# Optimization experiments

Hardware: AMD Instinct MI355X
Metric: run time of the kernel (lower is better)

Reference implementation:

```python
import jax, jax.numpy as jnp
import numpy as np
import math

HIDDEN = 2048
NUM_HEADS = 32
NUM_KV_HEADS = 8
HEAD_DIM = HIDDEN // NUM_HEADS
GROUPS = NUM_HEADS // NUM_KV_HEADS
B, S = 2, 2048


def setup_inputs() -> dict:
    key = jax.random.key(0)
    ks = jax.random.split(key, 9)
    sc = 1.0 / math.sqrt(HIDDEN)
    x = jax.random.normal(ks[0], (B, S, HIDDEN), dtype=jnp.float32)
    # causal mask: 1 where attention allowed, 0 where masked
    mask = jnp.tril(jnp.ones((S, S), dtype=jnp.int32))[None, None, :, :]
    Wq = jax.random.normal(ks[1], (HIDDEN, HIDDEN), dtype=jnp.float32) * sc
    bq = jnp.zeros((HIDDEN,), dtype=jnp.float32)
    Wk = jax.random.normal(ks[2], (NUM_KV_HEADS * HEAD_DIM, HIDDEN), dtype=jnp.float32) * sc
    bk = jnp.zeros((NUM_KV_HEADS * HEAD_DIM,), dtype=jnp.float32)
    Wv = jax.random.normal(ks[3], (NUM_KV_HEADS * HEAD_DIM, HIDDEN), dtype=jnp.float32) * sc
    bv = jnp.zeros((NUM_KV_HEADS * HEAD_DIM,), dtype=jnp.float32)
    Wo = jax.random.normal(ks[4], (HIDDEN, HIDDEN), dtype=jnp.float32) * sc
    bo = jnp.zeros((HIDDEN,), dtype=jnp.float32)
    return {"x": x, "mask": mask, "Wq": Wq, "bq": bq, "Wk": Wk, "bk": bk,
            "Wv": Wv, "bv": bv, "Wo": Wo, "bo": bo}


def reference(x, mask, Wq, bq, Wk, bk, Wv, bv, Wo, bo):
    b, s, _ = x.shape
    # projections (torch Linear: y = x @ W.T + b)
    Q = (x @ Wq.T + bq).reshape(b, s, NUM_HEADS, HEAD_DIM).transpose(0, 2, 1, 3)  # b h s d
    K = (x @ Wk.T + bk).reshape(b, s, NUM_KV_HEADS, HEAD_DIM).transpose(0, 2, 1, 3)
    V = (x @ Wv.T + bv).reshape(b, s, NUM_KV_HEADS, HEAD_DIM).transpose(0, 2, 1, 3)
    # repeat_kv expansion
    K = jnp.repeat(K, GROUPS, axis=1)  # b h s d
    V = jnp.repeat(V, GROUPS, axis=1)
    scores = jnp.einsum('bhqd,bhkd->bhqk', Q, K) / math.sqrt(HEAD_DIM)
    scores = jnp.where(mask == 0, jnp.float32(-jnp.inf), scores)
    w = jax.nn.softmax(scores, axis=-1)
    # dropout is identity in eval mode
    out = jnp.einsum('bhqk,bhkd->bhqd', w, V)
    out = out.transpose(0, 2, 1, 3).reshape(b, s, HIDDEN)
    return out @ Wo.T + bo
```

## Files before the change

### kernel.cpp

```cpp
#include <hip/hip_runtime.h>
#include <hip/hip_bf16.h>
#include <stdint.h>

#define HID   2048
#define SLEN  2048
#define NB    2
#define NHEADS 32
#define NKVH   8
#define HDIM   64
#define KVW    512

typedef __bf16 bf16_t;
typedef __bf16 bf16x2 __attribute__((ext_vector_type(2)));
typedef __bf16 bf16x4 __attribute__((ext_vector_type(4)));
typedef __bf16 bf16x8 __attribute__((ext_vector_type(8)));
typedef float  f32x4  __attribute__((ext_vector_type(4)));

__device__ __forceinline__ f32x4 mfma16(bf16x8 a, bf16x8 b, f32x4 c) {
  return __builtin_amdgcn_mfma_f32_16x16x32_bf16(a, b, c, 0, 0, 0);
}

__device__ __forceinline__ void gl2lds16(const bf16_t* g, bf16_t* l) {
  __builtin_amdgcn_global_load_lds(
      (const __attribute__((address_space(1))) void*)g,
      (__attribute__((address_space(3))) void*)l,
      16, 0, 0);
}

__device__ __forceinline__ float fast_exp2(float x) {
#if __has_builtin(__builtin_amdgcn_exp2f)
  return __builtin_amdgcn_exp2f(x);
#else
  return __expf(x * 0.69314718f);
#endif
}

__device__ __forceinline__ bf16x8 ld8(const bf16_t* p) {
  return *(const bf16x8*)p;
}
__device__ __forceinline__ bf16x8 ld8(const float* p) {
  f32x4 a = *(const f32x4*)p;
  f32x4 b = *(const f32x4*)(p + 4);
  bf16x8 r;
  r[0] = (bf16_t)a[0]; r[1] = (bf16_t)a[1]; r[2] = (bf16_t)a[2]; r[3] = (bf16_t)a[3];
  r[4] = (bf16_t)b[0]; r[5] = (bf16_t)b[1]; r[6] = (bf16_t)b[2]; r[7] = (bf16_t)b[3];
  return r;
}

__device__ __forceinline__ uint32_t pack2(float a, float b) {
  bf16x2 t; t[0] = (bf16_t)a; t[1] = (bf16_t)b;
  return __builtin_bit_cast(uint32_t, t);
}

__device__ __forceinline__ void st_c(bf16_t* p, float v) { *p = (bf16_t)v; }
__device__ __forceinline__ void st_c(float*  p, float v) { *p = v; }

__global__ __launch_bounds__(256) void cvt_kernel(
    const float* __restrict__ x,  const float* __restrict__ wq,
    const float* __restrict__ wk, const float* __restrict__ wv,
    const float* __restrict__ wo,
    const float* __restrict__ bq, const float* __restrict__ bk,
    const float* __restrict__ bv,
    bf16_t* xb, bf16_t* wqb, bf16_t* wkb, bf16_t* wvb, bf16_t* wob,
    float* bcat)
{
  if (blockIdx.y >= 5) {
    const float* fs; float* fd; size_t n;
    if (blockIdx.y == 5)      { fs = bq; fd = bcat;        n = HID; }
    else if (blockIdx.y == 6) { fs = bk; fd = bcat + HID;  n = KVW; }
    else                      { fs = bv; fd = bcat + HID + KVW; n = KVW; }
    const size_t stride4 = (size_t)gridDim.x * 256 * 4;
    for (size_t i = ((size_t)blockIdx.x * 256 + threadIdx.x) * 4; i < n; i += stride4)
      *(f32x4*)(fd + i) = *(const f32x4*)(fs + i);
    return;
  }
  const float* s; bf16_t* d; size_t n;
  switch (blockIdx.y) {
    case 0:  s = x;  d = xb;  n = (size_t)NB * SLEN * HID; break;
    case 1:  s = wq; d = wqb; n = (size_t)HID * HID; break;
    case 2:  s = wk; d = wkb; n = (size_t)KVW * HID; break;
    case 3:  s = wv; d = wvb; n = (size_t)KVW * HID; break;
    default: s = wo; d = wob; n = (size_t)HID * HID; break;
  }
  const size_t stride = (size_t)gridDim.x * 256 * 8;
  for (size_t i = ((size_t)blockIdx.x * 256 + threadIdx.x) * 8; i < n; i += stride)
    *(bf16x8*)(d + i) = ld8(s + i);
}

__device__ __forceinline__ bf16x8 ldfrag(const bf16_t* __restrict__ Lh, int r, int g) {
  return *(const bf16x8*)(Lh + r * 64 + ((g ^ (r & 7)) << 3));
}

template <int Q>
__device__ __forceinline__ void mfma_quad(const bf16x8 (&af)[2][2],
                                          const bf16x8 (&bfr)[4][2],
                                          f32x4 (&acc)[8][4]) {
#pragma unroll
  for (int ks = 0; ks < 2; ++ks)
#pragma unroll
    for (int i = 0; i < 2; ++i)
#pragma unroll
      for (int ni = 0; ni < 4; ++ni)
        acc[2 * Q + i][ni] = mfma16(af[i][ks], bfr[ni][ks], acc[2 * Q + i][ni]);
}

__device__ __forceinline__ void phase_barrier() {
  __builtin_amdgcn_s_barrier();
  asm volatile("" ::: "memory");
}

__device__ __forceinline__ void gemm256_core(
    const bf16_t* __restrict__ Ag,
    const bf16_t* __restrict__ Bg,
    bf16_t* __restrict__ lds, f32x4 (&acc)[8][4])
{
  const int tid  = threadIdx.x;
  const int lane = tid & 63;
  const int w    = tid >> 6;
  const int fr   = lane & 15;
  const int quad = lane >> 4;
  const int wr   = w >> 2;
  const int wc   = w & 3;
  const int rbB  = (wc & 1) * 64;

  bf16_t* A0 = lds;
  bf16_t* B0 = lds + 16384;
  bf16_t* A1 = lds + 32768;
  bf16_t* B1 = lds + 49152;
  const bf16_t* Ar0 = A0 + wr * 8192;
  const bf16_t* Br0 = B0 + (wc >> 1) * 8192;
  const bf16_t* Ar1 = A1 + wr * 8192;
  const bf16_t* Br1 = B1 + (wc >> 1) * 8192;

  const f32x4 z4 = {0.f, 0.f, 0.f, 0.f};
#pragma unroll
  for (int i = 0; i < 8; ++i)
#pragma unroll
    for (int j = 0; j < 4; ++j) acc[i][j] = z4;

  auto STAGE = [&](const bf16_t* __restrict__ Gp, bf16_t* __restrict__ Lh) {
#pragma unroll
    for (int j = 0; j < 2; ++j) {
      const int s = j * 512 + tid;
      const int r = s >> 3;
      const int g = (s & 7) ^ (r & 7);
      gl2lds16(Gp + (size_t)r * HID + g * 8, Lh + s * 8);
    }
  };

  STAGE(Bg,                  B0);
  STAGE(Bg + 128 * HID,      B0 + 8192);
  STAGE(Ag,                  A0);
  STAGE(Ag + 128 * HID,      A0 + 8192);
  STAGE(Bg + 64,             B1);
  STAGE(Bg + 128 * HID + 64, B1 + 8192);
  asm volatile("s_waitcnt vmcnt(4)" ::: "memory");
  phase_barrier();

  bf16x8 bfr[4][2], af[2][2];

#pragma unroll 1
  for (int it = 0; it < 16; ++it) {
    const bool more = (it < 15);
    const size_t k1 = (size_t)(2 * it + 1) * 64;
    const size_t k2 = (size_t)(2 * it + 2) * 64;
    const size_t k3 = (size_t)(2 * it + 3) * 64;

#pragma unroll
    for (int ni = 0; ni < 4; ++ni)
#pragma unroll
      for (int ks = 0; ks < 2; ++ks)
        bfr[ni][ks] = ldfrag(Br0, rbB + ni * 16 + fr, ks * 4 + quad);
#pragma unroll
    for (int i = 0; i < 2; ++i)
#pragma unroll
      for (int ks = 0; ks < 2; ++ks)
        af[i][ks] = ldfrag(Ar0, i * 16 + fr, ks * 4 + quad);
    STAGE(Ag + k1, A1);
    phase_barrier();
    asm volatile("s_waitcnt lgkmcnt(0)" ::: "memory");
    __builtin_amdgcn_s_setprio(1);
    mfma_quad<0>(af, bfr, acc);
    __builtin_amdgcn_s_setprio(0);
    phase_barrier();

#pragma unroll
    for (int i = 0; i < 2; ++i)
#pragma unroll
      for (int ks = 0; ks < 2; ++ks)
        af[i][ks] = ldfrag(Ar0, 32 + i * 16 + fr, ks * 4 + quad);
    STAGE(Ag + 128 * HID + k1, A1 + 8192);
    phase_barrier();
    asm volatile("s_waitcnt lgkmcnt(0)" ::: "memory");
    __builtin_amdgcn_s_setprio(1);
    mfma_quad<1>(af, bfr, acc);
    __builtin_amdgcn_s_setprio(0);
    phase_barrier();

#pragma unroll
    for (int i = 0; i < 2; ++i)
#pragma unroll
      for (int ks = 0; ks < 2; ++ks)
        af[i][ks] = ldfrag(Ar0, 64 + i * 16 + fr, ks * 4 + quad);
    if (more) STAGE(Bg + k2, B0);
    phase_barrier();
    asm volatile("s_waitcnt lgkmcnt(0)" ::: "memory");
    __builtin_amdgcn_s_setprio(1);
    mfma_quad<2>(af, bfr, acc);
    __builtin_amdgcn_s_setprio(0);
    phase_barrier();

#pragma unroll
    for (int i = 0; i < 2; ++i)
#pragma unroll
      for (int ks = 0; ks < 2; ++ks)
        af[i][ks] = ldfrag(Ar0, 96 + i * 16 + fr, ks * 4 + quad);
    if (more) STAGE(Bg + 128 * HID + k2, B0 + 8192);
    phase_barrier();
    asm volatile("s_waitcnt lgkmcnt(0)" ::: "memory");
    __builtin_amdgcn_s_setprio(1);
    mfma_quad<3>(af, bfr, acc);
    __builtin_amdgcn_s_setprio(0);
    if (more) { asm volatile("s_waitcnt vmcnt(4)" ::: "memory"); }
    else      { asm volatile("s_waitcnt vmcnt(0)" ::: "memory"); }
    phase_barrier();

#pragma unroll
    for (int ni = 0; ni < 4; ++ni)
#pragma unroll
      for (int ks = 0; ks < 2; ++ks)
        bfr[ni][ks] = ldfrag(Br1, rbB + ni * 16 + fr, ks * 4 + quad);
#pragma unroll
    for (int i = 0; i < 2; ++i)
#pragma unroll
      for (int ks = 0; ks < 2; ++ks)
        af[i][ks] = ldfrag(Ar1, i * 16 + fr, ks * 4 + quad);
    if (more) STAGE(Ag + k2, A0);
    phase_barrier();
    asm volatile("s_waitcnt lgkmcnt(0)" ::: "memory");
    __builtin_amdgcn_s_setprio(1);
    mfma_quad<0>(af, bfr, acc);
    __builtin_amdgcn_s_setprio(0);
    phase_barrier();

#pragma unroll
    for (int i = 0; i < 2; ++i)
#pragma unroll
      for (int ks = 0; ks < 2; ++ks)
        af[i][ks] = ldfrag(Ar1, 32 + i * 16 + fr, ks * 4 + quad);
    if (more) STAGE(Ag + 128 * HID + k2, A0 + 8192);
    phase_barrier();
    asm volatile("s_waitcnt lgkmcnt(0)" ::: "memory");
    __builtin_amdgcn_s_setprio(1);
    mfma_quad<1>(af, bfr, acc);
    __builtin_amdgcn_s_setprio(0);
    phase_barrier();

#pragma unroll
    for (int i = 0; i < 2; ++i)
#pragma unroll
      for (int ks = 0; ks < 2; ++ks)
        af[i][ks] = ldfrag(Ar1, 64 + i * 16 + fr, ks * 4 + quad);
    if (more) STAGE(Bg + k3, B1);
    phase_barrier();
    asm volatile("s_waitcnt lgkmcnt(0)" ::: "memory");
    __builtin_amdgcn_s_setprio(1);
    mfma_quad<2>(af, bfr, acc);
    __builtin_amdgcn_s_setprio(0);
    phase_barrier();

#pragma unroll
    for (int i = 0; i < 2; ++i)
#pragma unroll
      for (int ks = 0; ks < 2; ++ks)
        af[i][ks] = ldfrag(Ar1, 96 + i * 16 + fr, ks * 4 + quad);
    if (more) STAGE(Bg + 128 * HID + k3, B1 + 8192);
    phase_barrier();
    asm volatile("s_waitcnt lgkmcnt(0)" ::: "memory");
    __builtin_amdgcn_s_setprio(1);
    mfma_quad<3>(af, bfr, acc);
    __builtin_amdgcn_s_setprio(0);
    if (more) { asm volatile("s_waitcnt vmcnt(4)" ::: "memory"); }
    phase_barrier();
  }
}

__global__ __launch_bounds__(512, 2) void qkv8_kernel(
    const bf16_t* __restrict__ xb, const bf16_t* __restrict__ Wcat,
    const float* __restrict__ bcat,
    bf16_t* __restrict__ Qb, bf16_t* __restrict__ Kb, bf16_t* __restrict__ VbT)
{
  __shared__ __align__(16) bf16_t lds[65536];
  const int cb = blockIdx.x;
  const int mb = blockIdx.y;
  f32x4 acc[8][4];
  gemm256_core(xb + (size_t)mb * 256 * HID, Wcat + (size_t)cb * 256 * HID, lds, acc);

  const int tid = threadIdx.x, lane = tid & 63, w = tid >> 6;
  const int fr = lane & 15, quad = lane >> 4, wr = w >> 2, wc = w & 3;
#pragma unroll
  for (int ni = 0; ni < 4; ++ni) {
    const int gcol = cb * 256 + wc * 64 + ni * 16 + fr;
    const float bz = bcat[gcol];
#pragma unroll
    for (int mi = 0; mi < 8; ++mi) {
      const int grow = mb * 256 + wr * 128 + mi * 16 + quad * 4;
      if (cb < 8) {
#pragma unroll
        for (int r = 0; r < 4; ++r)
          Qb[(size_t)(grow + r) * HID + gcol] = (bf16_t)(acc[mi][ni][r] + bz);
      } else if (cb < 10) {
        const int kc = gcol - 2048;
#pragma unroll
        for (int r = 0; r < 4; ++r)
          Kb[(size_t)(grow + r) * KVW + kc] = (bf16_t)(acc[mi][ni][r] + bz);
      } else {
        const int vc = gcol - 2560;
        const int b = grow >> 11, s = grow & 2047;
        bf16x4 pk;
#pragma unroll
        for (int r = 0; r < 4; ++r) pk[r] = (bf16_t)(acc[mi][ni][r] + bz);
        *(bf16x4*)&VbT[((size_t)(b * NKVH + (vc >> 6)) * HDIM + (vc & 63)) * SLEN + s] = pk;
      }
    }
  }
}

__global__ __launch_bounds__(512, 2) void oproj8_kernel(
    const bf16_t* __restrict__ A, const bf16_t* __restrict__ Wob,
    const float* __restrict__ bo, float* __restrict__ out)
{
  __shared__ __align__(16) bf16_t lds[65536];
  const int cb = blockIdx.x;
  const int mb = blockIdx.y;
  f32x4 acc[8][4];
  gemm256_core(A + (size_t)mb * 256 * HID, Wob + (size_t)cb * 256 * HID, lds, acc);

  const int tid = threadIdx.x, lane = tid & 63, w = tid >> 6;
  const int fr = lane & 15, quad = lane >> 4, wr = w >> 2, wc = w & 3;
#pragma unroll
  for (int ni = 0; ni < 4; ++ni) {
    const int gcol = cb * 256 + wc * 64 + ni * 16 + fr;
    const float bz = bo[gcol];
#pragma unroll
    for (int mi = 0; mi < 8; ++mi) {
      const int grow = mb * 256 + wr * 128 + mi * 16 + quad * 4;
#pragma unroll
      for (int r = 0; r < 4; ++r)
        out[(size_t)(grow + r) * HID + gcol] = acc[mi][ni][r] + bz;
    }
  }
}

template <typename AT, typename CT>
__device__ __forceinline__ void gemm128_tile(
    const AT* __restrict__ Ap, int lda,
    const float* __restrict__ Wp, int ldw,
    const float* __restrict__ biasp,
    CT* __restrict__ Cp, int ldc,
    int K)
{
  __shared__ __align__(16) bf16_t Al[128 * 32];
  __shared__ __align__(16) bf16_t Bl[128 * 32];

  const int tid  = threadIdx.x;
  const int lane = tid & 63;
  const int w    = tid >> 6;
  const int fr   = lane & 15;
  const int quad = lane >> 4;
  const int wm   = (w >> 1) * 64;
  const int wn   = (w & 1) * 64;

  const f32x4 z4 = {0.f, 0.f, 0.f, 0.f};
  f32x4 acc[4][4];
  for (int i = 0; i < 4; ++i)
    for (int j = 0; j < 4; ++j) acc[i][j] = z4;

  const int c0    = w * 2;
  const int srow0 = lane >> 2;
  const int skc   = (lane & 3) * 8;

  for (int k0 = 0; k0 < K; k0 += 32) {
    bf16x8 av[2], bv[2];
    for (int t = 0; t < 2; ++t) {
      const int r = (c0 + t) * 16 + srow0;
      av[t] = ld8(Ap + (size_t)r * lda + k0 + skc);
      bv[t] = ld8(Wp + (size_t)r * ldw + k0 + skc);
    }
    for (int t = 0; t < 2; ++t) {
      const int c = c0 + t;
      *(bf16x8*)&Al[c * 512 + lane * 8] = av[t];
      *(bf16x8*)&Bl[c * 512 + lane * 8] = bv[t];
    }
    __syncthreads();
    bf16x8 af[4], bfr[4];
    for (int mi = 0; mi < 4; ++mi)
      af[mi] = *(const bf16x8*)&Al[(wm + mi * 16 + fr) * 32 + quad * 8];
    for (int ni = 0; ni < 4; ++ni)
      bfr[ni] = *(const bf16x8*)&Bl[(wn + ni * 16 + fr) * 32 + quad * 8];
    for (int mi = 0; mi < 4; ++mi)
      for (int ni = 0; ni < 4; ++ni)
        acc[mi][ni] = mfma16(af[mi], bfr[ni], acc[mi][ni]);
    __syncthreads();
  }

  for (int ni = 0; ni < 4; ++ni) {
    const int col = wn + ni * 16 + fr;
    const float bz = biasp[col];
    for (int mi = 0; mi < 4; ++mi) {
      const int r0 = wm + mi * 16 + quad * 4;
      for (int r = 0; r < 4; ++r)
        st_c(Cp + (size_t)(r0 + r) * ldc + col, acc[mi][ni][r] + bz);
    }
  }
}

__global__ __launch_bounds__(256) void qkv_kernel(
    const float* __restrict__ x,
    const float* __restrict__ Wq, const float* __restrict__ bq,
    const float* __restrict__ Wk, const float* __restrict__ bk,
    const float* __restrict__ Wv, const float* __restrict__ bv,
    bf16_t* Qb, bf16_t* Kb, bf16_t* Vb)
{
  const int nb = blockIdx.x;
  const int mb = blockIdx.y;
  const float* W; const float* bias; bf16_t* C; int ldc;
  if (nb < 16)      { W = Wq + (size_t)nb * 128 * HID;  bias = bq + nb * 128;
                      C = Qb + nb * 128; ldc = HID; }
  else if (nb < 20) { const int j = nb - 16;
                      W = Wk + (size_t)j * 128 * HID;   bias = bk + j * 128;
                      C = Kb + j * 128; ldc = KVW; }
  else              { const int j = nb - 20;
                      W = Wv + (size_t)j * 128 * HID;   bias = bv + j * 128;
                      C = Vb + j * 128; ldc = KVW; }
  gemm128_tile<float, bf16_t>(x + (size_t)mb * 128 * HID, HID, W, HID, bias,
                              C + (size_t)mb * 128 * ldc, ldc, HID);
}

__global__ __launch_bounds__(256) void oproj_kernel(
    const bf16_t* __restrict__ A, const float* __restrict__ Wo,
    const float* __restrict__ bo, float* out)
{
  const int nb = blockIdx.x, mb = blockIdx.y;
  gemm128_tile<bf16_t, float>(A + (size_t)mb * 128 * HID, HID,
                              Wo + (size_t)nb * 128 * HID, HID,
                              bo + nb * 128,
                              out + (size_t)mb * 128 * HID + nb * 128, HID, HID);
}

__global__ __launch_bounds__(256) void vtrans_kernel(
    const bf16_t* __restrict__ Vb, bf16_t* __restrict__ VbT)
{
  __shared__ bf16_t T[64][72];
  const int st = blockIdx.x, kvh = blockIdx.y, b = blockIdx.z;
  const int tid = threadIdx.x;
  {
    const int row = tid >> 2;
    const int c16 = (tid & 3) * 16;
    const bf16_t* src =
        Vb + ((size_t)b * SLEN + st * 64 + row) * KVW + kvh * HDIM + c16;
    *(bf16x8*)&T[row][c16]     = *(const bf16x8*)(src);
    *(bf16x8*)&T[row][c16 + 8] = *(const bf16x8*)(src + 8);
  }
  __syncthreads();
  {
    const int d  = tid >> 2;
    const int sc = (tid & 3) * 16;
    bf16_t tmp[16];
    for (int j = 0; j < 16; ++j) tmp[j] = T[sc + j][d];
    bf16_t* dst = VbT + ((size_t)(b * NKVH + kvh) * HDIM + d) * SLEN + st * 64 + sc;
    *(bf16x8*)dst       = *(bf16x8*)&tmp[0];
    *(bf16x8*)(dst + 8) = *(bf16x8*)&tmp[8];
  }
}

__global__ __launch_bounds__(256, 4) void attn_kernel(
    const bf16_t* Q, const bf16_t* __restrict__ Kg,
    const bf16_t* __restrict__ VT, bf16_t* O)
{
  const int bid = blockIdx.x;
  const int xcd = bid & 7;
  const int j   = bid >> 3;
  const int kvh = xcd;
  const int b   = j >> 6;
  const int rem = j & 63;
  const int h   = kvh * 4 + (rem & 3);
  const int pid = rem >> 2;

  const int tid  = threadIdx.x;
  const int lane = tid & 63;
  const int w    = tid >> 6;
  const int fr   = lane & 15;
  const int quad = lane >> 4;

  __shared__ __align__(16) bf16_t KL[8192];
  __shared__ __align__(16) bf16_t VtL[8192];

  const size_t qbase = (size_t)b * SLEN;
  const bf16_t* VTh = VT + (size_t)(b * NKVH + kvh) * HDIM * SLEN;

  const int sig = ((quad & 1) << 1) | ((quad >> 1) & 1);
  const int fsw = (fr >> 1) & 3;
  const bool oddq = (quad & 1);

  bf16x8 ones8;
  {
    const bf16_t o1 = (bf16_t)(fr == 0 ? 1.0f : 0.0f);
#pragma unroll
    for (int j2 = 0; j2 < 8; ++j2) ones8[j2] = o1;
  }

  for (int half = 0; half < 2; ++half) {
    const int qt = half ? (31 - pid) : pid;
    const int q0 = qt * 64;

    bf16x8 qf[2];
#pragma unroll
    for (int ks = 0; ks < 2; ++ks)
      qf[ks] = *(const bf16x8*)&Q[(qbase + q0 + w * 16 + fr) * HID
                                  + h * HDIM + ks * 32 + quad * 8];

    const f32x4 z4 = {0.f, 0.f, 0.f, 0.f};
    f32x4 o_acc[4];
    f32x4 o_l = z4;
#pragma unroll
    for (int di = 0; di < 4; ++di) o_acc[di] = z4;

    const int ktmax = qt >> 1;
    const int qloc  = (qt & 1) * 64 + w * 16 + fr;

    for (int kt = 0; kt <= ktmax; ++kt) {
      const size_t krow0 = qbase + (size_t)kt * 128;

#pragma unroll
      for (int jj = 0; jj < 4; ++jj) {
        const int s  = jj * 256 + tid;
        const int ks = s >> 9, kr = (s >> 2) & 127, c8 = (s & 3) ^ ((kr >> 1) & 3);
        gl2lds16(&Kg[(krow0 + kr) * KVW + kvh * HDIM + ks * 32 + c8 * 8],
                 &KL[s * 8]);
      }
#pragma unroll
      for (int jj = 0; jj < 4; ++jj) {
        const int idx = jj * 256 + tid;
        const int kb = idx >> 8, d = (idx >> 2) & 63, c8 = (idx & 3) ^ ((d >> 1) & 3);
        gl2lds16(&VTh[(size_t)d * SLEN + kt * 128 + kb * 32 + c8 * 8],
                 &VtL[idx * 8]);
      }
      __syncthreads();

      f32x4 s8[8];
#pragma unroll
      for (int ki = 0; ki < 8; ++ki) s8[ki] = z4;
#pragma unroll
      for (int ks = 0; ks < 2; ++ks)
#pragma unroll
        for (int ki = 0; ki < 8; ++ki) {
          bf16x8 kf = *(const bf16x8*)&KL[ks * 4096 + (ki * 16 + fr) * 32
                                          + ((quad ^ fsw) << 3)];
          s8[ki] = mfma16(kf, qf[ks], s8[ki]);
        }

      const float C2 = 0.18033688f;
      const bool diag = (kt == ktmax);

#pragma unroll
      for (int m = 0; m < 4; ++m) {
        float pe[8];
#pragma unroll
        for (int ki2 = 0; ki2 < 2; ++ki2) {
          const int ki = 2 * m + ki2;
#pragma unroll
          for (int r = 0; r < 4; ++r) {
            float p = fast_exp2(s8[ki][r] * C2);
            if (diag && (ki * 16 + quad * 4 + r > qloc)) p = 0.f;
            pe[ki2 * 4 + r] = p;
          }
        }
        uint32_t pw0 = pack2(pe[0], pe[1]);
        uint32_t pw1 = pack2(pe[2], pe[3]);
        uint32_t pw2 = pack2(pe[4], pe[5]);
        uint32_t pw3 = pack2(pe[6], pe[7]);
        uint32_t x0 = oddq ? pw0 : pw2;
        uint32_t x1 = oddq ? pw1 : pw3;
        uint32_t r0 = (uint32_t)__shfl_xor((int)x0, 16);
        uint32_t r1 = (uint32_t)__shfl_xor((int)x1, 16);
        union { uint32_t u[4]; bf16x8 v; } pb;
        pb.u[0] = oddq ? r0 : pw0;
        pb.u[1] = oddq ? r1 : pw1;
        pb.u[2] = oddq ? pw2 : r0;
        pb.u[3] = oddq ? pw3 : r1;

        o_l = mfma16(pb.v, ones8, o_l);
#pragma unroll
        for (int di = 0; di < 4; ++di) {
          bf16x8 vf = *(const bf16x8*)&VtL[m * 2048 + (di * 16 + fr) * 32
                                           + ((sig ^ fsw) << 3)];
          o_acc[di] = mfma16(pb.v, vf, o_acc[di]);
        }
      }
      __syncthreads();
    }

#pragma unroll
    for (int r = 0; r < 4; ++r) {
      const float l  = __shfl(o_l[r], lane & 48);
      const float rl = 1.f / l;
      const size_t qg = qbase + q0 + w * 16 + quad * 4 + r;
#pragma unroll
      for (int di = 0; di < 4; ++di)
        O[qg * HID + h * HDIM + di * 16 + fr] = (bf16_t)(o_acc[di][r] * rl);
    }
  }
}

extern "C" void kernel_launch(void* const* d_in, const int* in_sizes, int n_in,
                              void* d_out, int out_size, void* d_ws, size_t ws_size,
                              hipStream_t stream) {
  const float* x  = (const float*)d_in[0];
  const float* Wq = (const float*)d_in[2];
  const float* bq = (const float*)d_in[3];
  const float* Wk = (const float*)d_in[4];
  const float* bk = (const float*)d_in[5];
  const float* Wv = (const float*)d_in[6];
  const float* bv = (const float*)d_in[7];
  const float* Wo = (const float*)d_in[8];
  const float* bo = (const float*)d_in[9];
  float* out = (float*)d_out;

  const size_t M = (size_t)NB * SLEN;
  dim3 blk(256, 1, 1);

  const size_t needA = (M * HID
                        + (size_t)HID * HID
                        + (size_t)KVW * HID
                        + (size_t)KVW * HID
                        + (size_t)HID * HID
                        + M * HID
                        + M * KVW
                        + M * KVW) * 2
                       + (size_t)(HID + 2 * KVW) * sizeof(float);
  if (ws_size >= needA) {
    bf16_t* xb  = (bf16_t*)d_ws;
    bf16_t* Wqb = xb  + M * HID;
    bf16_t* Wkb = Wqb + (size_t)HID * HID;
    bf16_t* Wvb = Wkb + (size_t)KVW * HID;
    bf16_t* Wob = Wvb + (size_t)KVW * HID;
    bf16_t* Qb  = Wob + (size_t)HID * HID;
    bf16_t* Kb  = Qb  + M * HID;
    bf16_t* VbT = Kb  + M * KVW;
    float*  bcat = (float*)(VbT + M * KVW);

    cvt_kernel<<<dim3(1024, 8, 1), blk, 0, stream>>>(
        x, Wq, Wk, Wv, Wo, bq, bk, bv, xb, Wqb, Wkb, Wvb, Wob, bcat);
    qkv8_kernel<<<dim3(12, 16, 1), dim3(512, 1, 1), 0, stream>>>(
        xb, Wqb, bcat, Qb, Kb, VbT);
    attn_kernel<<<dim3(1024, 1, 1), blk, 0, stream>>>(Qb, Kb, VbT, Qb);
    oproj8_kernel<<<dim3(8, 16, 1), dim3(512, 1, 1), 0, stream>>>(
        Qb, Wob, bo, out);
  } else {
    bf16_t* Qb  = (bf16_t*)d_ws;
    bf16_t* Kb  = Qb + M * KVW * 0 + M * HID;
    bf16_t* Vb  = Kb + M * KVW;
    bf16_t* VbT = Vb + M * KVW;

    qkv_kernel<<<dim3(24, 32, 1), blk, 0, stream>>>(x, Wq, bq, Wk, bk, Wv, bv, Qb, Kb, Vb);
    vtrans_kernel<<<dim3(32, 8, 2), blk, 0, stream>>>(Vb, VbT);
    attn_kernel<<<dim3(1024, 1, 1), blk, 0, stream>>>(Qb, Kb, VbT, Qb);
    oproj_kernel<<<dim3(16, 32, 1), blk, 0, stream>>>(Qb, Wo, bo, out);
  }
}
```

Before: 320.6 us.

## Double-buffer K/V tiles in attention with 512-thread blocks and staged output stores

The attention kernel now uses 512-thread blocks that each own a 128-row query tile, halving the grid. K and V^T tiles are double-buffered in one 64 KB LDS array, so the next tile's global-to-LDS load overlaps the current tile's MFMA work, with one barrier per iteration instead of two. MFMA sections are wrapped in s_setprio, and the output is staged through LDS so global writes are coalesced 16-element vectors. The larger LDS footprint and block size lower occupancy, and the coarser causal tiles add some masked work on the diagonal.

```diff
diff --git a/kernel.cpp b/kernel.cpp
--- a/kernel.cpp
+++ b/kernel.cpp
@@ -474,16 +474,15 @@
   }
 }
 
-__global__ __launch_bounds__(256, 4) void attn_kernel(
+__global__ __launch_bounds__(512, 4) void attn_kernel(
     const bf16_t* Q, const bf16_t* __restrict__ Kg,
     const bf16_t* __restrict__ VT, bf16_t* O)
 {
   const int bid = blockIdx.x;
-  const int xcd = bid & 7;
-  const int j   = bid >> 3;
-  const int kvh = xcd;
-  const int b   = j >> 6;
-  const int rem = j & 63;
+  const int kvh = bid & 7;
+  const int jb  = bid >> 3;
+  const int b   = jb >> 5;
+  const int rem = jb & 31;
   const int h   = kvh * 4 + (rem & 3);
   const int pid = rem >> 2;
 
@@ -493,8 +492,7 @@
   const int fr   = lane & 15;
   const int quad = lane >> 4;
 
-  __shared__ __align__(16) bf16_t KL[8192];
-  __shared__ __align__(16) bf16_t VtL[8192];
+  __shared__ __align__(16) bf16_t lds[32768];
 
   const size_t qbase = (size_t)b * SLEN;
   const bf16_t* VTh = VT + (size_t)(b * NKVH + kvh) * HDIM * SLEN;
@@ -510,9 +508,28 @@
     for (int j2 = 0; j2 < 8; ++j2) ones8[j2] = o1;
   }
 
+  auto STAGE_KV = [&](int kt, bf16_t* KL) {
+    const size_t krow0 = qbase + (size_t)kt * 128;
+    bf16_t* VtL = KL + 8192;
+#pragma unroll
+    for (int jj = 0; jj < 2; ++jj) {
+      const int s  = jj * 512 + tid;
+      const int ks = s >> 9, kr = (s >> 2) & 127, c8 = (s & 3) ^ ((kr >> 1) & 3);
+      gl2lds16(&Kg[(krow0 + kr) * KVW + kvh * HDIM + ks * 32 + c8 * 8],
+               &KL[s * 8]);
+    }
+#pragma unroll
+    for (int jj = 0; jj < 2; ++jj) {
+      const int idx = jj * 512 + tid;
+      const int kb = idx >> 8, d = (idx >> 2) & 63, c8 = (idx & 3) ^ ((d >> 1) & 3);
+      gl2lds16(&VTh[(size_t)d * SLEN + kt * 128 + kb * 32 + c8 * 8],
+               &VtL[idx * 8]);
+    }
+  };
+
   for (int half = 0; half < 2; ++half) {
-    const int qt = half ? (31 - pid) : pid;
-    const int q0 = qt * 64;
+    const int qt = half ? (15 - pid) : pid;
+    const int q0 = qt * 128;
 
     bf16x8 qf[2];
 #pragma unroll
@@ -526,31 +543,23 @@
 #pragma unroll
     for (int di = 0; di < 4; ++di) o_acc[di] = z4;
 
-    const int ktmax = qt >> 1;
-    const int qloc  = (qt & 1) * 64 + w * 16 + fr;
-
+    const int ktmax = qt;
+    const int qloc  = w * 16 + fr;
+
+    STAGE_KV(0, lds);
+    asm volatile("s_waitcnt vmcnt(0)" ::: "memory");
+    phase_barrier();
+
+    int cur = 0;
     for (int kt = 0; kt <= ktmax; ++kt) {
-      const size_t krow0 = qbase + (size_t)kt * 128;
-
-#pragma unroll
-      for (int jj = 0; jj < 4; ++jj) {
-        const int s  = jj * 256 + tid;
-        const int ks = s >> 9, kr = (s >> 2) & 127, c8 = (s & 3) ^ ((kr >> 1) & 3);
-        gl2lds16(&Kg[(krow0 + kr) * KVW + kvh * HDIM + ks * 32 + c8 * 8],
-                 &KL[s * 8]);
-      }
-#pragma unroll
-      for (int jj = 0; jj < 4; ++jj) {
-        const int idx = jj * 256 + tid;
-        const int kb = idx >> 8, d = (idx >> 2) & 63, c8 = (idx & 3) ^ ((d >> 1) & 3);
-        gl2lds16(&VTh[(size_t)d * SLEN + kt * 128 + kb * 32 + c8 * 8],
-                 &VtL[idx * 8]);
-      }
-      __syncthreads();
+      bf16_t* KL  = lds + cur * 16384;
+      bf16_t* VtL = KL + 8192;
+      if (kt < ktmax) STAGE_KV(kt + 1, lds + (cur ^ 1) * 16384);
 
       f32x4 s8[8];
 #pragma unroll
       for (int ki = 0; ki < 8; ++ki) s8[ki] = z4;
+      __builtin_amdgcn_s_setprio(1);
 #pragma unroll
       for (int ks = 0; ks < 2; ++ks)
 #pragma unroll
@@ -559,6 +568,7 @@
                                           + ((quad ^ fsw) << 3)];
           s8[ki] = mfma16(kf, qf[ks], s8[ki]);
         }
+      __builtin_amdgcn_s_setprio(0);
 
       const float C2 = 0.18033688f;
       const bool diag = (kt == ktmax);
@@ -590,6 +600,7 @@
         pb.u[2] = oddq ? pw2 : r0;
         pb.u[3] = oddq ? pw3 : r1;
 
+        __builtin_amdgcn_s_setprio(1);
         o_l = mfma16(pb.v, ones8, o_l);
 #pragma unroll
         for (int di = 0; di < 4; ++di) {
@@ -597,19 +608,36 @@
                                            + ((sig ^ fsw) << 3)];
           o_acc[di] = mfma16(pb.v, vf, o_acc[di]);
         }
+        __builtin_amdgcn_s_setprio(0);
       }
-      __syncthreads();
-    }
-
+
+      asm volatile("s_waitcnt vmcnt(0)" ::: "memory");
+      phase_barrier();
+      cur ^= 1;
+    }
+
+    bf16_t* OB = lds;
 #pragma unroll
     for (int r = 0; r < 4; ++r) {
       const float l  = __shfl(o_l[r], lane & 48);
       const float rl = 1.f / l;
-      const size_t qg = qbase + q0 + w * 16 + quad * 4 + r;
+      const int q = w * 16 + quad * 4 + r;
 #pragma unroll
       for (int di = 0; di < 4; ++di)
-        O[qg * HID + h * HDIM + di * 16 + fr] = (bf16_t)(o_acc[di][r] * rl);
-    }
+        OB[q * 64 + di * 16 + fr] = (bf16_t)(o_acc[di][r] * rl);
+    }
+    asm volatile("s_waitcnt lgkmcnt(0)" ::: "memory");
+    phase_barrier();
+    {
+      const int row = tid >> 2;
+      const int seg = tid & 3;
+      bf16x8 v0 = *(const bf16x8*)&OB[row * 64 + seg * 16];
+      bf16x8 v1 = *(const bf16x8*)&OB[row * 64 + seg * 16 + 8];
+      bf16_t* dst = &O[(qbase + q0 + row) * HID + h * HDIM + seg * 16];
+      *(bf16x8*)dst       = v0;
+      *(bf16x8*)(dst + 8) = v1;
+    }
+    phase_barrier();
   }
 }
 
@@ -654,18 +682,18 @@
         x, Wq, Wk, Wv, Wo, bq, bk, bv, xb, Wqb, Wkb, Wvb, Wob, bcat);
     qkv8_kernel<<<dim3(12, 16, 1), dim3(512, 1, 1), 0, stream>>>(
         xb, Wqb, bcat, Qb, Kb, VbT);
-    attn_kernel<<<dim3(1024, 1, 1), blk, 0, stream>>>(Qb, Kb, VbT, Qb);
+    attn_kernel<<<dim3(512, 1, 1), dim3(512, 1, 1), 0, stream>>>(Qb, Kb, VbT, Qb);
     oproj8_kernel<<<dim3(8, 16, 1), dim3(512, 1, 1), 0, stream>>>(
         Qb, Wob, bo, out);
   } else {
     bf16_t* Qb  = (bf16_t*)d_ws;
-    bf16_t* Kb  = Qb + M * KVW * 0 + M * HID;
+    bf16_t* Kb  = Qb + M * HID;
     bf16_t* Vb  = Kb + M * KVW;
     bf16_t* VbT = Vb + M * KVW;
 
     qkv_kernel<<<dim3(24, 32, 1), blk, 0, stream>>>(x, Wq, bq, Wk, bk, Wv, bv, Qb, Kb, Vb);
     vtrans_kernel<<<dim3(32, 8, 2), blk, 0, stream>>>(Vb, VbT);
-    attn_kernel<<<dim3(1024, 1, 1), blk, 0, stream>>>(Qb, Kb, VbT, Qb);
+    attn_kernel<<<dim3(512, 1, 1), dim3(512, 1, 1), 0, stream>>>(Qb, Kb, VbT, Qb);
     oproj_kernel<<<dim3(16, 32, 1), blk, 0, stream>>>(Qb, Wo, bo, out);
   }
 }
```

Result: faster. 299.8 us (-6.5%).
